# Performance work log

Measured on AMD Instinct MI355X. Metric: run time of the kernel, lower is better.

Reference implementation:

```python
import jax, jax.numpy as jnp
import numpy as np

N_NODES = 25000
N_EDGES = 400000
N = 2          # per-node group dim (h.size(1))
IN_DIM = 64
HEADS = 4
HEAD_DIM = 16  # out_dim; HEADS*HEAD_DIM == IN_DIM here


def setup_inputs() -> dict:
    key = jax.random.key(0)
    ks = jax.random.split(key, 8)
    w_scale = 1.0 / np.sqrt(IN_DIM)
    return {
        "h": jax.random.normal(ks[0], (N_NODES, N, IN_DIM), jnp.float32),
        "e": jax.random.normal(ks[1], (N_EDGES, N, IN_DIM), jnp.float32),
        "W_Q": jax.random.normal(ks[2], (IN_DIM, HEADS * HEAD_DIM), jnp.float32) * w_scale,
        "W_K": jax.random.normal(ks[3], (IN_DIM, HEADS * HEAD_DIM), jnp.float32) * w_scale,
        "W_V": jax.random.normal(ks[4], (IN_DIM, HEADS * HEAD_DIM), jnp.float32) * w_scale,
        "W_repe": jax.random.normal(ks[5], (IN_DIM, HEADS * HEAD_DIM), jnp.float32) * w_scale,
        "src": jax.random.randint(ks[6], (N_EDGES,), 0, N_NODES, jnp.int32),
        "dst": jax.random.randint(ks[7], (N_EDGES,), 0, N_NODES, jnp.int32),
    }


def reference(h, e, W_Q, W_K, W_V, W_repe, src, dst):
    n_nodes, Nd, C = h.shape
    E = src.shape[0]
    # node-side projection Q_h: [n_nodes, N, H, D]
    Q_h = (h @ W_Q).reshape(n_nodes, Nd, HEADS, HEAD_DIM)
    # edge-side bias repe_e: [E, N, H, D]
    repe_e = (e @ W_repe).reshape(E, Nd, HEADS, HEAD_DIM)
    # compute_diff: relu(src - dst) on raw features  [E, N, C]
    diff = jax.nn.relu(h[src] - h[dst])
    k_diff = (diff @ W_K).reshape(E, Nd, HEADS, HEAD_DIM)
    v_diff = (diff @ W_V).reshape(E, Nd, HEADS, HEAD_DIM)
    # dst_cosim_diff: scale = ||k_diff|| * ||Q_h[dst]|| + 1e-6 (norm over last dim, keepdim)
    q_dst = Q_h[dst]  # [E, N, H, D]
    scale = (jnp.linalg.norm(k_diff, axis=-1, keepdims=True)
             * jnp.linalg.norm(q_dst, axis=-1, keepdims=True)) + 1e-6
    score = q_dst * k_diff * scale + repe_e
    msg = score * v_diff
    # update_all(copy_edge, max) -> segment max over dst; zero-degree nodes get 0 (DGL convention)
    h_out = jax.ops.segment_max(msg, dst, num_segments=n_nodes)
    h_out = jnp.where(jnp.isneginf(h_out), jnp.zeros((), h_out.dtype), h_out)
    return h_out
```

## Files before the change

kernel.cpp:

```cpp
#include <hip/hip_runtime.h>
#include <stdint.h>

#define N_NODES 25000
#define N_EDGES 400000

typedef __attribute__((ext_vector_type(8))) short short8;
typedef __attribute__((ext_vector_type(4))) float f32x4;

#define MFMA16(a, b, c) __builtin_amdgcn_mfma_f32_16x16x32_bf16((a), (b), (c), 0, 0, 0)

__device__ __forceinline__ short bf16r(float x) {
    unsigned u = __float_as_uint(x);
    u += 0x7FFFu + ((u >> 16) & 1u);
    return (short)(u >> 16);
}
__device__ __forceinline__ short bfr(float x) {
    return (short)((__float_as_uint(x) + 0x8000u) >> 16);
}

#define DPP_ADD(x, ctrl) \
    ((x) + __int_as_float(__builtin_amdgcn_update_dpp(0, __float_as_int(x), (ctrl), 0xF, 0xF, true)))
__device__ __forceinline__ float red16(float x) {
    x = DPP_ADD(x, 0xB1);
    x = DPP_ADD(x, 0x4E);
    x = DPP_ADD(x, 0x141);
    x = DPP_ADD(x, 0x140);
    return x;
}

__device__ __forceinline__ short8 load_bfrag(const float* __restrict__ W,
                                             int colbase, int lane, int khalf) {
    const int n = colbase + (lane & 15);
    const int k0 = khalf * 32 + ((lane >> 4) << 3);
    short8 f;
    #pragma unroll
    for (int j = 0; j < 8; ++j) f[j] = bf16r(W[(k0 + j) * 64 + n]);
    return f;
}

__device__ __forceinline__ short8 afrag(const short* S, int lane, int khalf) {
    return *(const short8*)&S[(lane & 15) * 72 + khalf * 32 + ((lane >> 4) << 3)];
}

__global__ __launch_bounds__(256) void zero_counts_kernel(int* __restrict__ counts) {
    const int i = blockIdx.x * 256 + threadIdx.x;
    if (i < N_NODES) counts[i] = 0;
}

__global__ __launch_bounds__(256) void hist_kernel(const int* __restrict__ dst,
                                                   int* __restrict__ counts) {
    const int i = blockIdx.x * 256 + threadIdx.x;
    if (i < N_EDGES) atomicAdd(&counts[dst[i]], 1);
}

#define BPT 98
__global__ __launch_bounds__(256) void scan_kernel(const int* __restrict__ counts,
                                                   int* __restrict__ offsets,
                                                   int* __restrict__ cursor) {
    __shared__ int part[256];
    const int t = threadIdx.x;
    const int base = t * BPT;
    int s = 0;
    for (int j = 0; j < BPT; ++j) {
        const int idx = base + j;
        if (idx < N_NODES) s += counts[idx];
    }
    part[t] = s;
    __syncthreads();
    for (int d = 1; d < 256; d <<= 1) {
        const int add = (t >= d) ? part[t - d] : 0;
        __syncthreads();
        part[t] += add;
        __syncthreads();
    }
    int run = (t > 0) ? part[t - 1] : 0;
    for (int j = 0; j < BPT; ++j) {
        const int idx = base + j;
        if (idx < N_NODES) {
            offsets[idx] = run;
            cursor[idx]  = run;
            run += counts[idx];
        }
    }
    if (t == 255) offsets[N_NODES] = part[255];
}

__global__ __launch_bounds__(256) void scatter_kernel(
    const int* __restrict__ src, const int* __restrict__ dst,
    int* __restrict__ cursor, int* __restrict__ perm, int* __restrict__ srcs) {
    const int i = blockIdx.x * 256 + threadIdx.x;
    if (i < N_EDGES) {
        const int d = dst[i];
        const int pos = atomicAdd(&cursor[d], 1);
        perm[pos] = i;
        srcs[pos] = src[i];
    }
}

__global__ __launch_bounds__(256) void q_mfma_kernel(
    const float* __restrict__ h, const float* __restrict__ Wq,
    const float* __restrict__ Wk, const float* __restrict__ Wv,
    const float* __restrict__ Wr, float* __restrict__ Q, short8* __restrict__ fw)
{
    __shared__ short sH[64 * 72];
    const int t = threadIdx.x;
    const int lane = t & 63, w = t >> 6;
    const int wcol = w << 4;
    const int ln = lane & 15, lq = lane >> 4;
    const int base = blockIdx.x * 64;

    const short8 b0 = load_bfrag(Wq, wcol, lane, 0);
    const short8 b1 = load_bfrag(Wq, wcol, lane, 1);

    {
        const int r = t >> 2, c4 = (t & 3) << 4;
        int row = base + r; if (row > 49999) row = 49999;
        const float4* p = (const float4*)&h[row * 64 + c4];
        short tmp[16];
        #pragma unroll
        for (int i = 0; i < 4; ++i) {
            float4 x = p[i];
            tmp[4*i+0] = bf16r(x.x); tmp[4*i+1] = bf16r(x.y);
            tmp[4*i+2] = bf16r(x.z); tmp[4*i+3] = bf16r(x.w);
        }
        *(short8*)&sH[r * 72 + c4]     = *(short8*)&tmp[0];
        *(short8*)&sH[r * 72 + c4 + 8] = *(short8*)&tmp[8];
    }
    __syncthreads();

    #pragma unroll
    for (int m = 0; m < 4; ++m) {
        const short* Sm = &sH[(m << 4) * 72];
        short8 a0 = afrag(Sm, lane, 0);
        short8 a1 = afrag(Sm, lane, 1);
        f32x4 acc = {0.f, 0.f, 0.f, 0.f};
        acc = MFMA16(a0, b0, acc);
        acc = MFMA16(a1, b1, acc);
        #pragma unroll
        for (int reg = 0; reg < 4; ++reg) {
            const int row = base + (m << 4) + (lq << 2) + reg;
            if (row < 50000) Q[row * 64 + wcol + ln] = acc[reg];
        }
    }

    if (blockIdx.x == 0) {
        fw[(w * 6 + 0) * 64 + lane] = load_bfrag(Wk, wcol, lane, 0);
        fw[(w * 6 + 1) * 64 + lane] = load_bfrag(Wk, wcol, lane, 1);
        fw[(w * 6 + 2) * 64 + lane] = load_bfrag(Wv, wcol, lane, 0);
        fw[(w * 6 + 3) * 64 + lane] = load_bfrag(Wv, wcol, lane, 1);
        fw[(w * 6 + 4) * 64 + lane] = load_bfrag(Wr, wcol, lane, 0);
        fw[(w * 6 + 5) * 64 + lane] = load_bfrag(Wr, wcol, lane, 1);
    }
}

__global__ __launch_bounds__(256, 2) void edge_wave_kernel(
    const float* __restrict__ h, const float* __restrict__ e,
    const float* __restrict__ Q, const int* __restrict__ srcs,
    const int* __restrict__ perm, const int* __restrict__ offsets,
    const short8* __restrict__ fw, float* __restrict__ out)
{
    __shared__ short sAll[4][2304];
    const int t = threadIdx.x;
    const int lane = t & 63, w = t >> 6;
    const int v = (blockIdx.x << 2) + w;
    short* SD = &sAll[w][0];
    short* SE = &sAll[w][1152];

    const int off0 = offsets[v];
    const int off1 = offsets[v + 1];
    const int deg  = off1 - off0;

    if (deg == 0) {
        out[(v << 7) + lane]      = 0.0f;
        out[(v << 7) + 64 + lane] = 0.0f;
        return;
    }

    const int ln = lane & 15, lq = lane >> 4;

    short8 bK0[4], bK1[4], bV0[4], bV1[4], bR0[4], bR1[4];
    #pragma unroll
    for (int hd = 0; hd < 4; ++hd) {
        bK0[hd] = fw[(hd * 6 + 0) * 64 + lane];
        bK1[hd] = fw[(hd * 6 + 1) * 64 + lane];
        bV0[hd] = fw[(hd * 6 + 2) * 64 + lane];
        bV1[hd] = fw[(hd * 6 + 3) * 64 + lane];
        bR0[hd] = fw[(hd * 6 + 4) * 64 + lane];
        bR1[hd] = fw[(hd * 6 + 5) * 64 + lane];
    }

    float q0[4], q1[4], qn0[4], qn1[4];
    #pragma unroll
    for (int hd = 0; hd < 4; ++hd) {
        q0[hd] = Q[(v << 7) + (hd << 4) + ln];
        q1[hd] = Q[(v << 7) + 64 + (hd << 4) + ln];
        qn0[hd] = sqrtf(red16(q0[hd] * q0[hd]));
        qn1[hd] = sqrtf(red16(q1[hd] * q1[hd]));
    }

    const int r = lane >> 2;
    const int cq = (lane & 3) << 4;
    const int n_r = r & 1;

    float4 xd[4];
    {
        const float4* pd = (const float4*)&h[(((v << 1) + n_r) << 6) + cq];
        xd[0] = pd[0]; xd[1] = pd[1]; xd[2] = pd[2]; xd[3] = pd[3];
    }

    const float NEG_INF = __uint_as_float(0xFF800000u);
    float rm0[4] = {NEG_INF, NEG_INF, NEG_INF, NEG_INF};
    float rm1[4] = {NEG_INF, NEG_INF, NEG_INF, NEG_INF};

    const int nch = (deg + 7) >> 3;
    for (int c = 0; c < nch; ++c) {
        int eidx = off0 + (c << 3) + (r >> 1);
        if (eidx > off1 - 1) eidx = off1 - 1;
        const int ed = perm[eidx];
        const int s  = srcs[eidx];
        const float4* ps = (const float4*)&h[(((s  << 1) + n_r) << 6) + cq];
        const float4* pe = (const float4*)&e[(((ed << 1) + n_r) << 6) + cq];

        short tmd[16], tme[16];
        #pragma unroll
        for (int i = 0; i < 4; ++i) {
            const float4 xs = ps[i], xe = pe[i];
            tmd[4*i+0] = bfr(fmaxf(xs.x - xd[i].x, 0.f));
            tmd[4*i+1] = bfr(fmaxf(xs.y - xd[i].y, 0.f));
            tmd[4*i+2] = bfr(fmaxf(xs.z - xd[i].z, 0.f));
            tmd[4*i+3] = bfr(fmaxf(xs.w - xd[i].w, 0.f));
            tme[4*i+0] = bfr(xe.x); tme[4*i+1] = bfr(xe.y);
            tme[4*i+2] = bfr(xe.z); tme[4*i+3] = bfr(xe.w);
        }
        *(short8*)&SD[r * 72 + cq]     = *(short8*)&tmd[0];
        *(short8*)&SD[r * 72 + cq + 8] = *(short8*)&tmd[8];
        *(short8*)&SE[r * 72 + cq]     = *(short8*)&tme[0];
        *(short8*)&SE[r * 72 + cq + 8] = *(short8*)&tme[8];

        __builtin_amdgcn_wave_barrier();

        const short8 a0 = afrag(SD, lane, 0);
        const short8 a1 = afrag(SD, lane, 1);
        const short8 g0 = afrag(SE, lane, 0);
        const short8 g1 = afrag(SE, lane, 1);

        #pragma unroll
        for (int hd = 0; hd < 4; ++hd) {
            f32x4 aK = {0.f, 0.f, 0.f, 0.f}, aV = aK, aR = aK;
            aK = MFMA16(a0, bK0[hd], aK); aK = MFMA16(a1, bK1[hd], aK);
            aV = MFMA16(a0, bV0[hd], aV); aV = MFMA16(a1, bV1[hd], aV);
            aR = MFMA16(g0, bR0[hd], aR); aR = MFMA16(g1, bR1[hd], aR);

            #pragma unroll
            for (int reg = 0; reg < 4; ++reg) {
                const int rl   = (lq << 2) + reg;
                const int eloc = rl >> 1;
                const int n2   = reg & 1;
                const bool valid = ((c << 3) + eloc) < deg;
                const float kk = aK[reg];
                const float sk = red16(kk * kk);
                const float scale = sqrtf(sk) * (n2 ? qn1[hd] : qn0[hd]) + 1e-6f;
                const float qv = n2 ? q1[hd] : q0[hd];
                float msg = (qv * kk * scale + aR[reg]) * aV[reg];
                msg = valid ? msg : NEG_INF;
                if (n2) rm1[hd] = fmaxf(rm1[hd], msg);
                else    rm0[hd] = fmaxf(rm0[hd], msg);
            }
        }
        __builtin_amdgcn_wave_barrier();
    }

    #pragma unroll
    for (int hd = 0; hd < 4; ++hd) {
        rm0[hd] = fmaxf(rm0[hd], __shfl_xor(rm0[hd], 16));
        rm0[hd] = fmaxf(rm0[hd], __shfl_xor(rm0[hd], 32));
        rm1[hd] = fmaxf(rm1[hd], __shfl_xor(rm1[hd], 16));
        rm1[hd] = fmaxf(rm1[hd], __shfl_xor(rm1[hd], 32));
    }
    const float o0 = (lq == 0) ? rm0[0] : (lq == 1) ? rm0[1] : (lq == 2) ? rm0[2] : rm0[3];
    const float o1 = (lq == 0) ? rm1[0] : (lq == 1) ? rm1[1] : (lq == 2) ? rm1[2] : rm1[3];
    out[(v << 7) + lane]      = o0;
    out[(v << 7) + 64 + lane] = o1;
}

extern "C" void kernel_launch(void* const* d_in, const int* in_sizes, int n_in,
                              void* d_out, int out_size, void* d_ws, size_t ws_size,
                              hipStream_t stream) {
    const float* h  = (const float*)d_in[0];
    const float* e  = (const float*)d_in[1];
    const float* Wq = (const float*)d_in[2];
    const float* Wk = (const float*)d_in[3];
    const float* Wv = (const float*)d_in[4];
    const float* Wr = (const float*)d_in[5];
    const int*   src = (const int*)d_in[6];
    const int*   dst = (const int*)d_in[7];
    float* out = (float*)d_out;

    float* Q       = (float*)d_ws;
    int*   counts  = (int*)d_ws + 3200000;
    int*   offsets = (int*)d_ws + 3225000;
    int*   cursor  = (int*)d_ws + 3250008;
    int*   perm    = (int*)d_ws + 3275008;
    int*   srcs    = (int*)d_ws + 3675008;
    short8* fw     = (short8*)((int*)d_ws + 4075008);

    zero_counts_kernel<<<98, 256, 0, stream>>>(counts);
    hist_kernel<<<1563, 256, 0, stream>>>(dst, counts);
    scan_kernel<<<1, 256, 0, stream>>>(counts, offsets, cursor);
    scatter_kernel<<<1563, 256, 0, stream>>>(src, dst, cursor, perm, srcs);
    q_mfma_kernel<<<782, 256, 0, stream>>>(h, Wq, Wk, Wv, Wr, Q, fw);
    edge_wave_kernel<<<6250, 256, 0, stream>>>(h, e, Q, srcs, perm, offsets, fw, out);
}
```

Baseline: 512.9 us.

## Split edge work into per-wave 8-edge chunks with atomic max reduction

Replaces the one-wave-per-node loop with one wave per 8-edge chunk, using a chunk descriptor list built after the scan. Each chunk loads its fragments directly into registers instead of staging them through LDS, and reduces into the output with an atomicMax on order-preserving mapped floats. A final pass unmaps the values and zeroes empty nodes. This targets load imbalance from varying node degree and raises occupancy, at the cost of extra launches, redundant Q/dst reloads per chunk, and global atomics.

Measured after the change: 533.1 us. 1.04x slower.

```diff
diff --git a/kernel.cpp b/kernel.cpp
--- a/kernel.cpp
+++ b/kernel.cpp
@@ -3,6 +3,8 @@
 
 #define N_NODES 25000
 #define N_EDGES 400000
+#define OUT_ELEMS 3200000
+#define MAX_CHUNKS 72000
 
 typedef __attribute__((ext_vector_type(8))) short short8;
 typedef __attribute__((ext_vector_type(4))) float f32x4;
@@ -28,6 +30,12 @@
     return x;
 }
 
+__device__ __forceinline__ unsigned fmap(float x) {
+    const unsigned u = __float_as_uint(x);
+    return ((int)u >= 0) ? (u | 0x80000000u) : ~u;
+}
+#define MAPPED_NEG_INF 0x007FFFFFu
+
 __device__ __forceinline__ short8 load_bfrag(const float* __restrict__ W,
                                              int colbase, int lane, int khalf) {
     const int n = colbase + (lane & 15);
@@ -42,8 +50,10 @@
     return *(const short8*)&S[(lane & 15) * 72 + khalf * 32 + ((lane >> 4) << 3)];
 }
 
-__global__ __launch_bounds__(256) void zero_counts_kernel(int* __restrict__ counts) {
+__global__ __launch_bounds__(256) void init_kernel(unsigned* __restrict__ out_u,
+                                                   int* __restrict__ counts) {
     const int i = blockIdx.x * 256 + threadIdx.x;
+    out_u[i] = MAPPED_NEG_INF;
     if (i < N_NODES) counts[i] = 0;
 }
 
@@ -56,33 +66,64 @@
 #define BPT 98
 __global__ __launch_bounds__(256) void scan_kernel(const int* __restrict__ counts,
                                                    int* __restrict__ offsets,
-                                                   int* __restrict__ cursor) {
-    __shared__ int part[256];
+                                                   int* __restrict__ cursor,
+                                                   int* __restrict__ chunkoff) {
+    __shared__ int pd[256];
+    __shared__ int pc[256];
     const int t = threadIdx.x;
     const int base = t * BPT;
-    int s = 0;
-    for (int j = 0; j < BPT; ++j) {
-        const int idx = base + j;
-        if (idx < N_NODES) s += counts[idx];
-    }
-    part[t] = s;
-    __syncthreads();
-    for (int d = 1; d < 256; d <<= 1) {
-        const int add = (t >= d) ? part[t - d] : 0;
-        __syncthreads();
-        part[t] += add;
-        __syncthreads();
-    }
-    int run = (t > 0) ? part[t - 1] : 0;
+    int sd = 0, sc = 0;
     for (int j = 0; j < BPT; ++j) {
         const int idx = base + j;
         if (idx < N_NODES) {
-            offsets[idx] = run;
-            cursor[idx]  = run;
-            run += counts[idx];
-        }
-    }
-    if (t == 255) offsets[N_NODES] = part[255];
+            const int d = counts[idx];
+            sd += d;
+            sc += (d + 7) >> 3;
+        }
+    }
+    pd[t] = sd; pc[t] = sc;
+    __syncthreads();
+    for (int d = 1; d < 256; d <<= 1) {
+        const int ad = (t >= d) ? pd[t - d] : 0;
+        const int ac = (t >= d) ? pc[t - d] : 0;
+        __syncthreads();
+        pd[t] += ad; pc[t] += ac;
+        __syncthreads();
+    }
+    int rd = (t > 0) ? pd[t - 1] : 0;
+    int rc = (t > 0) ? pc[t - 1] : 0;
+    for (int j = 0; j < BPT; ++j) {
+        const int idx = base + j;
+        if (idx < N_NODES) {
+            offsets[idx]  = rd;
+            cursor[idx]   = rd;
+            chunkoff[idx] = rc;
+            const int d = counts[idx];
+            rd += d;
+            rc += (d + 7) >> 3;
+        }
+    }
+    if (t == 255) { offsets[N_NODES] = pd[255]; chunkoff[N_NODES] = pc[255]; }
+}
+
+__global__ __launch_bounds__(256) void fill_kernel(const int* __restrict__ offsets,
+                                                   const int* __restrict__ chunkoff,
+                                                   int2* __restrict__ chunk_desc) {
+    const int v = blockIdx.x * 256 + threadIdx.x;
+    if (v < N_NODES) {
+        const int off0 = offsets[v];
+        const int deg  = offsets[v + 1] - off0;
+        const int nch  = (deg + 7) >> 3;
+        const int co   = chunkoff[v];
+        for (int c = 0; c < nch; ++c) {
+            int nval = deg - (c << 3);
+            if (nval > 8) nval = 8;
+            int2 d;
+            d.x = v;
+            d.y = (off0 + (c << 3)) | (nval << 24);
+            chunk_desc[co + c] = d;
+        }
+    }
 }
 
 __global__ __launch_bounds__(256) void scatter_kernel(
@@ -153,30 +194,31 @@
     }
 }
 
-__global__ __launch_bounds__(256, 2) void edge_wave_kernel(
+__global__ __launch_bounds__(256, 4) void edge_chunk_kernel(
     const float* __restrict__ h, const float* __restrict__ e,
     const float* __restrict__ Q, const int* __restrict__ srcs,
-    const int* __restrict__ perm, const int* __restrict__ offsets,
-    const short8* __restrict__ fw, float* __restrict__ out)
+    const int* __restrict__ perm, const int* __restrict__ chunkoff,
+    const int2* __restrict__ chunk_desc, const short8* __restrict__ fw,
+    unsigned* __restrict__ out_u)
 {
-    __shared__ short sAll[4][2304];
     const int t = threadIdx.x;
-    const int lane = t & 63, w = t >> 6;
-    const int v = (blockIdx.x << 2) + w;
-    short* SD = &sAll[w][0];
-    short* SE = &sAll[w][1152];
-
-    const int off0 = offsets[v];
-    const int off1 = offsets[v + 1];
-    const int deg  = off1 - off0;
-
-    if (deg == 0) {
-        out[(v << 7) + lane]      = 0.0f;
-        out[(v << 7) + 64 + lane] = 0.0f;
-        return;
-    }
+    const int lane = t & 63;
+    const int g = (blockIdx.x << 2) + (t >> 6);
+    if (g >= chunkoff[N_NODES]) return;
+
+    const int2 dsc = chunk_desc[g];
+    const int v    = dsc.x;
+    const int base = dsc.y & 0xFFFFFF;
+    const int nval = dsc.y >> 24;
 
     const int ln = lane & 15, lq = lane >> 4;
+    const int eloc = ln >> 1, nr = ln & 1;
+    const int k0 = lq << 3;
+
+    const int elc = (eloc < nval - 1) ? eloc : (nval - 1);
+    const int ei  = base + elc;
+    const int ed  = perm[ei];
+    const int s   = srcs[ei];
 
     short8 bK0[4], bK1[4], bV0[4], bV1[4], bR0[4], bR1[4];
     #pragma unroll
@@ -189,6 +231,35 @@
         bR1[hd] = fw[(hd * 6 + 5) * 64 + lane];
     }
 
+    const float* __restrict__ hs  = &h[((s  << 1) + nr) << 6];
+    const float* __restrict__ hdp = &h[((v  << 1) + nr) << 6];
+    const float* __restrict__ ep  = &e[((ed << 1) + nr) << 6];
+
+    short8 afr[2], gfr[2];
+    #pragma unroll
+    for (int half = 0; half < 2; ++half) {
+        const int cb = (half << 5) + k0;
+        const float4 s0 = *(const float4*)&hs[cb];
+        const float4 s1 = *(const float4*)&hs[cb + 4];
+        const float4 d0 = *(const float4*)&hdp[cb];
+        const float4 d1 = *(const float4*)&hdp[cb + 4];
+        const float4 e0 = *(const float4*)&ep[cb];
+        const float4 e1 = *(const float4*)&ep[cb + 4];
+        short8 ta, tg;
+        ta[0] = bfr(fmaxf(s0.x - d0.x, 0.f));
+        ta[1] = bfr(fmaxf(s0.y - d0.y, 0.f));
+        ta[2] = bfr(fmaxf(s0.z - d0.z, 0.f));
+        ta[3] = bfr(fmaxf(s0.w - d0.w, 0.f));
+        ta[4] = bfr(fmaxf(s1.x - d1.x, 0.f));
+        ta[5] = bfr(fmaxf(s1.y - d1.y, 0.f));
+        ta[6] = bfr(fmaxf(s1.z - d1.z, 0.f));
+        ta[7] = bfr(fmaxf(s1.w - d1.w, 0.f));
+        tg[0] = bfr(e0.x); tg[1] = bfr(e0.y); tg[2] = bfr(e0.z); tg[3] = bfr(e0.w);
+        tg[4] = bfr(e1.x); tg[5] = bfr(e1.y); tg[6] = bfr(e1.z); tg[7] = bfr(e1.w);
+        afr[half] = ta;
+        gfr[half] = tg;
+    }
+
     float q0[4], q1[4], qn0[4], qn1[4];
     #pragma unroll
     for (int hd = 0; hd < 4; ++hd) {
@@ -198,76 +269,32 @@
         qn1[hd] = sqrtf(red16(q1[hd] * q1[hd]));
     }
 
-    const int r = lane >> 2;
-    const int cq = (lane & 3) << 4;
-    const int n_r = r & 1;
-
-    float4 xd[4];
-    {
-        const float4* pd = (const float4*)&h[(((v << 1) + n_r) << 6) + cq];
-        xd[0] = pd[0]; xd[1] = pd[1]; xd[2] = pd[2]; xd[3] = pd[3];
-    }
-
     const float NEG_INF = __uint_as_float(0xFF800000u);
     float rm0[4] = {NEG_INF, NEG_INF, NEG_INF, NEG_INF};
     float rm1[4] = {NEG_INF, NEG_INF, NEG_INF, NEG_INF};
 
-    const int nch = (deg + 7) >> 3;
-    for (int c = 0; c < nch; ++c) {
-        int eidx = off0 + (c << 3) + (r >> 1);
-        if (eidx > off1 - 1) eidx = off1 - 1;
-        const int ed = perm[eidx];
-        const int s  = srcs[eidx];
-        const float4* ps = (const float4*)&h[(((s  << 1) + n_r) << 6) + cq];
-        const float4* pe = (const float4*)&e[(((ed << 1) + n_r) << 6) + cq];
-
-        short tmd[16], tme[16];
+    #pragma unroll
+    for (int hd = 0; hd < 4; ++hd) {
+        f32x4 aK = {0.f, 0.f, 0.f, 0.f}, aV = aK, aR = aK;
+        aK = MFMA16(afr[0], bK0[hd], aK); aK = MFMA16(afr[1], bK1[hd], aK);
+        aV = MFMA16(afr[0], bV0[hd], aV); aV = MFMA16(afr[1], bV1[hd], aV);
+        aR = MFMA16(gfr[0], bR0[hd], aR); aR = MFMA16(gfr[1], bR1[hd], aR);
+
         #pragma unroll
-        for (int i = 0; i < 4; ++i) {
-            const float4 xs = ps[i], xe = pe[i];
-            tmd[4*i+0] = bfr(fmaxf(xs.x - xd[i].x, 0.f));
-            tmd[4*i+1] = bfr(fmaxf(xs.y - xd[i].y, 0.f));
-            tmd[4*i+2] = bfr(fmaxf(xs.z - xd[i].z, 0.f));
-            tmd[4*i+3] = bfr(fmaxf(xs.w - xd[i].w, 0.f));
-            tme[4*i+0] = bfr(xe.x); tme[4*i+1] = bfr(xe.y);
-            tme[4*i+2] = bfr(xe.z); tme[4*i+3] = bfr(xe.w);
-        }
-        *(short8*)&SD[r * 72 + cq]     = *(short8*)&tmd[0];
-        *(short8*)&SD[r * 72 + cq + 8] = *(short8*)&tmd[8];
-        *(short8*)&SE[r * 72 + cq]     = *(short8*)&tme[0];
-        *(short8*)&SE[r * 72 + cq + 8] = *(short8*)&tme[8];
-
-        __builtin_amdgcn_wave_barrier();
-
-        const short8 a0 = afrag(SD, lane, 0);
-        const short8 a1 = afrag(SD, lane, 1);
-        const short8 g0 = afrag(SE, lane, 0);
-        const short8 g1 = afrag(SE, lane, 1);
-
-        #pragma unroll
-        for (int hd = 0; hd < 4; ++hd) {
-            f32x4 aK = {0.f, 0.f, 0.f, 0.f}, aV = aK, aR = aK;
-            aK = MFMA16(a0, bK0[hd], aK); aK = MFMA16(a1, bK1[hd], aK);
-            aV = MFMA16(a0, bV0[hd], aV); aV = MFMA16(a1, bV1[hd], aV);
-            aR = MFMA16(g0, bR0[hd], aR); aR = MFMA16(g1, bR1[hd], aR);
-
-            #pragma unroll
-            for (int reg = 0; reg < 4; ++reg) {
-                const int rl   = (lq << 2) + reg;
-                const int eloc = rl >> 1;
-                const int n2   = reg & 1;
-                const bool valid = ((c << 3) + eloc) < deg;
-                const float kk = aK[reg];
-                const float sk = red16(kk * kk);
-                const float scale = sqrtf(sk) * (n2 ? qn1[hd] : qn0[hd]) + 1e-6f;
-                const float qv = n2 ? q1[hd] : q0[hd];
-                float msg = (qv * kk * scale + aR[reg]) * aV[reg];
-                msg = valid ? msg : NEG_INF;
-                if (n2) rm1[hd] = fmaxf(rm1[hd], msg);
-                else    rm0[hd] = fmaxf(rm0[hd], msg);
-            }
-        }
-        __builtin_amdgcn_wave_barrier();
+        for (int reg = 0; reg < 4; ++reg) {
+            const int rl = (lq << 2) + reg;
+            const int el = rl >> 1;
+            const int n2 = reg & 1;
+            const bool valid = el < nval;
+            const float kk = aK[reg];
+            const float sk = red16(kk * kk);
+            const float scale = sqrtf(sk) * (n2 ? qn1[hd] : qn0[hd]) + 1e-6f;
+            const float qv = n2 ? q1[hd] : q0[hd];
+            float msg = (qv * kk * scale + aR[reg]) * aV[reg];
+            msg = valid ? msg : NEG_INF;
+            if (n2) rm1[hd] = fmaxf(rm1[hd], msg);
+            else    rm0[hd] = fmaxf(rm0[hd], msg);
+        }
     }
 
     #pragma unroll
@@ -279,8 +306,25 @@
     }
     const float o0 = (lq == 0) ? rm0[0] : (lq == 1) ? rm0[1] : (lq == 2) ? rm0[2] : rm0[3];
     const float o1 = (lq == 0) ? rm1[0] : (lq == 1) ? rm1[1] : (lq == 2) ? rm1[2] : rm1[3];
-    out[(v << 7) + lane]      = o0;
-    out[(v << 7) + 64 + lane] = o1;
+    atomicMax(&out_u[(v << 7) + lane],      fmap(o0));
+    atomicMax(&out_u[(v << 7) + 64 + lane], fmap(o1));
+}
+
+__global__ __launch_bounds__(256) void final_kernel(unsigned* __restrict__ io) {
+    const int i = blockIdx.x * 256 + threadIdx.x;
+    uint4* p = (uint4*)io;
+    uint4 m = p[i];
+    unsigned a, b, c, d;
+    a = (m.x & 0x80000000u) ? (m.x ^ 0x80000000u) : ~m.x;
+    b = (m.y & 0x80000000u) ? (m.y ^ 0x80000000u) : ~m.y;
+    c = (m.z & 0x80000000u) ? (m.z ^ 0x80000000u) : ~m.z;
+    d = (m.w & 0x80000000u) ? (m.w ^ 0x80000000u) : ~m.w;
+    if (a == 0xFF800000u) a = 0u;
+    if (b == 0xFF800000u) b = 0u;
+    if (c == 0xFF800000u) c = 0u;
+    if (d == 0xFF800000u) d = 0u;
+    m.x = a; m.y = b; m.z = c; m.w = d;
+    p[i] = m;
 }
 
 extern "C" void kernel_launch(void* const* d_in, const int* in_sizes, int n_in,
@@ -296,18 +340,23 @@
     const int*   dst = (const int*)d_in[7];
     float* out = (float*)d_out;
 
-    float* Q       = (float*)d_ws;
-    int*   counts  = (int*)d_ws + 3200000;
-    int*   offsets = (int*)d_ws + 3225000;
-    int*   cursor  = (int*)d_ws + 3250008;
-    int*   perm    = (int*)d_ws + 3275008;
-    int*   srcs    = (int*)d_ws + 3675008;
-    short8* fw     = (short8*)((int*)d_ws + 4075008);
-
-    zero_counts_kernel<<<98, 256, 0, stream>>>(counts);
+    float* Q        = (float*)d_ws;
+    int*   counts   = (int*)d_ws + 3200000;
+    int*   offsets  = (int*)d_ws + 3225000;
+    int*   cursor   = (int*)d_ws + 3250008;
+    int*   perm     = (int*)d_ws + 3275008;
+    int*   srcs     = (int*)d_ws + 3675008;
+    short8* fw      = (short8*)((int*)d_ws + 4075008);
+    int*   chunkoff = (int*)d_ws + 4081152;
+    int2*  chunk_desc = (int2*)((int*)d_ws + 4106154);
+
+    init_kernel<<<12500, 256, 0, stream>>>((unsigned*)out, counts);
     hist_kernel<<<1563, 256, 0, stream>>>(dst, counts);
-    scan_kernel<<<1, 256, 0, stream>>>(counts, offsets, cursor);
+    scan_kernel<<<1, 256, 0, stream>>>(counts, offsets, cursor, chunkoff);
+    fill_kernel<<<98, 256, 0, stream>>>(offsets, chunkoff, chunk_desc);
     scatter_kernel<<<1563, 256, 0, stream>>>(src, dst, cursor, perm, srcs);
     q_mfma_kernel<<<782, 256, 0, stream>>>(h, Wq, Wk, Wv, Wr, Q, fw);
-    edge_wave_kernel<<<6250, 256, 0, stream>>>(h, e, Q, srcs, perm, offsets, fw, out);
-}
+    edge_chunk_kernel<<<17969, 256, 0, stream>>>(h, e, Q, srcs, perm,
+                                                 chunkoff, chunk_desc, fw, (unsigned*)out);
+    final_kernel<<<3125, 256, 0, stream>>>((unsigned*)out);
+}
```

## Split edge kernel into edge-parallel message pass and CSR-ordered max reduce

Applied to the files above, without the earlier changes.

The per-destination-node edge loop is replaced by an edge-parallel kernel. It processes 8 edges per wave in original order, reading e coalesced, and writes bf16-packed messages into CSR positions. A separate reduce kernel then takes the segment max per node. The Q norm is folded into Q in the projection kernel, and the 1e-6 epsilon term is dropped. This removes load imbalance from skewed degrees and the scattered e reads, but adds an intermediate message buffer round trip (about 51 MB of bf16) and a bf16 rounding of the messages.

Measured after the change: 534.9 us. +4.3%, slower.

```diff
diff --git a/kernel.cpp b/kernel.cpp
--- a/kernel.cpp
+++ b/kernel.cpp
@@ -85,15 +85,13 @@
     if (t == 255) offsets[N_NODES] = part[255];
 }
 
-__global__ __launch_bounds__(256) void scatter_kernel(
-    const int* __restrict__ src, const int* __restrict__ dst,
-    int* __restrict__ cursor, int* __restrict__ perm, int* __restrict__ srcs) {
+__global__ __launch_bounds__(256) void scatter_pos_kernel(
+    const int* __restrict__ dst, int* __restrict__ cursor,
+    int* __restrict__ csr_pos) {
     const int i = blockIdx.x * 256 + threadIdx.x;
     if (i < N_EDGES) {
-        const int d = dst[i];
-        const int pos = atomicAdd(&cursor[d], 1);
-        perm[pos] = i;
-        srcs[pos] = src[i];
+        const int pos = atomicAdd(&cursor[dst[i]], 1);
+        csr_pos[i] = pos;
     }
 }
 
@@ -138,8 +136,9 @@
         acc = MFMA16(a1, b1, acc);
         #pragma unroll
         for (int reg = 0; reg < 4; ++reg) {
+            const float qn = sqrtf(red16(acc[reg] * acc[reg]));
             const int row = base + (m << 4) + (lq << 2) + reg;
-            if (row < 50000) Q[row * 64 + wcol + ln] = acc[reg];
+            if (row < 50000) Q[row * 64 + wcol + ln] = acc[reg] * qn;
         }
     }
 
@@ -153,134 +152,138 @@
     }
 }
 
-__global__ __launch_bounds__(256, 2) void edge_wave_kernel(
+__global__ __launch_bounds__(256, 4) void edge_msg_kernel(
     const float* __restrict__ h, const float* __restrict__ e,
-    const float* __restrict__ Q, const int* __restrict__ srcs,
-    const int* __restrict__ perm, const int* __restrict__ offsets,
-    const short8* __restrict__ fw, float* __restrict__ out)
+    const float* __restrict__ QQ, const int* __restrict__ src,
+    const int* __restrict__ dst, const int* __restrict__ csr_pos,
+    const short8* __restrict__ fw, uint2* __restrict__ msg)
 {
-    __shared__ short sAll[4][2304];
     const int t = threadIdx.x;
-    const int lane = t & 63, w = t >> 6;
-    const int v = (blockIdx.x << 2) + w;
-    short* SD = &sAll[w][0];
-    short* SE = &sAll[w][1152];
-
-    const int off0 = offsets[v];
-    const int off1 = offsets[v + 1];
-    const int deg  = off1 - off0;
-
-    if (deg == 0) {
-        out[(v << 7) + lane]      = 0.0f;
-        out[(v << 7) + 64 + lane] = 0.0f;
-        return;
-    }
-
+    const int lane = t & 63;
+    const int g = (blockIdx.x << 2) + (t >> 6);
+    const int g8 = g << 3;
     const int ln = lane & 15, lq = lane >> 4;
-
-    short8 bK0[4], bK1[4], bV0[4], bV1[4], bR0[4], bR1[4];
+    const int eloc = ln >> 1, nr = ln & 1;
+    const int k0 = lq << 3;
+
+    const int sA = src[g8 + eloc];
+    const int dA = dst[g8 + eloc];
+    const float* __restrict__ hs  = &h[((sA << 1) + nr) << 6];
+    const float* __restrict__ hdp = &h[((dA << 1) + nr) << 6];
+    const float* __restrict__ ep  = &e[(((g8 + eloc) << 1) + nr) << 6];
+
+    short8 afr[2], gfr[2];
+    #pragma unroll
+    for (int half = 0; half < 2; ++half) {
+        const int cb = (half << 5) + k0;
+        const float4 s0 = *(const float4*)&hs[cb];
+        const float4 s1 = *(const float4*)&hs[cb + 4];
+        const float4 d0 = *(const float4*)&hdp[cb];
+        const float4 d1 = *(const float4*)&hdp[cb + 4];
+        const float4 e0 = *(const float4*)&ep[cb];
+        const float4 e1 = *(const float4*)&ep[cb + 4];
+        short8 ta, tg;
+        ta[0] = bfr(fmaxf(s0.x - d0.x, 0.f));
+        ta[1] = bfr(fmaxf(s0.y - d0.y, 0.f));
+        ta[2] = bfr(fmaxf(s0.z - d0.z, 0.f));
+        ta[3] = bfr(fmaxf(s0.w - d0.w, 0.f));
+        ta[4] = bfr(fmaxf(s1.x - d1.x, 0.f));
+        ta[5] = bfr(fmaxf(s1.y - d1.y, 0.f));
+        ta[6] = bfr(fmaxf(s1.z - d1.z, 0.f));
+        ta[7] = bfr(fmaxf(s1.w - d1.w, 0.f));
+        tg[0] = bfr(e0.x); tg[1] = bfr(e0.y); tg[2] = bfr(e0.z); tg[3] = bfr(e0.w);
+        tg[4] = bfr(e1.x); tg[5] = bfr(e1.y); tg[6] = bfr(e1.z); tg[7] = bfr(e1.w);
+        afr[half] = ta;
+        gfr[half] = tg;
+    }
+
+    const int e0i = g8 + (lq << 1), e1i = e0i + 1;
+    const int d0 = dst[e0i], d1 = dst[e1i];
+    const int p0 = csr_pos[e0i], p1 = csr_pos[e1i];
+
+    float qv_e0n0[4], qv_e0n1[4], qv_e1n0[4], qv_e1n1[4];
     #pragma unroll
     for (int hd = 0; hd < 4; ++hd) {
-        bK0[hd] = fw[(hd * 6 + 0) * 64 + lane];
-        bK1[hd] = fw[(hd * 6 + 1) * 64 + lane];
-        bV0[hd] = fw[(hd * 6 + 2) * 64 + lane];
-        bV1[hd] = fw[(hd * 6 + 3) * 64 + lane];
-        bR0[hd] = fw[(hd * 6 + 4) * 64 + lane];
-        bR1[hd] = fw[(hd * 6 + 5) * 64 + lane];
-    }
-
-    float q0[4], q1[4], qn0[4], qn1[4];
+        qv_e0n0[hd] = QQ[(d0 << 7) + (hd << 4) + ln];
+        qv_e0n1[hd] = QQ[(d0 << 7) + 64 + (hd << 4) + ln];
+        qv_e1n0[hd] = QQ[(d1 << 7) + (hd << 4) + ln];
+        qv_e1n1[hd] = QQ[(d1 << 7) + 64 + (hd << 4) + ln];
+    }
+
+    f32x4 aK[4], aV[4], aR[4];
     #pragma unroll
     for (int hd = 0; hd < 4; ++hd) {
-        q0[hd] = Q[(v << 7) + (hd << 4) + ln];
-        q1[hd] = Q[(v << 7) + 64 + (hd << 4) + ln];
-        qn0[hd] = sqrtf(red16(q0[hd] * q0[hd]));
-        qn1[hd] = sqrtf(red16(q1[hd] * q1[hd]));
-    }
-
-    const int r = lane >> 2;
-    const int cq = (lane & 3) << 4;
-    const int n_r = r & 1;
-
-    float4 xd[4];
-    {
-        const float4* pd = (const float4*)&h[(((v << 1) + n_r) << 6) + cq];
-        xd[0] = pd[0]; xd[1] = pd[1]; xd[2] = pd[2]; xd[3] = pd[3];
-    }
-
-    const float NEG_INF = __uint_as_float(0xFF800000u);
-    float rm0[4] = {NEG_INF, NEG_INF, NEG_INF, NEG_INF};
-    float rm1[4] = {NEG_INF, NEG_INF, NEG_INF, NEG_INF};
-
-    const int nch = (deg + 7) >> 3;
-    for (int c = 0; c < nch; ++c) {
-        int eidx = off0 + (c << 3) + (r >> 1);
-        if (eidx > off1 - 1) eidx = off1 - 1;
-        const int ed = perm[eidx];
-        const int s  = srcs[eidx];
-        const float4* ps = (const float4*)&h[(((s  << 1) + n_r) << 6) + cq];
-        const float4* pe = (const float4*)&e[(((ed << 1) + n_r) << 6) + cq];
-
-        short tmd[16], tme[16];
-        #pragma unroll
-        for (int i = 0; i < 4; ++i) {
-            const float4 xs = ps[i], xe = pe[i];
-            tmd[4*i+0] = bfr(fmaxf(xs.x - xd[i].x, 0.f));
-            tmd[4*i+1] = bfr(fmaxf(xs.y - xd[i].y, 0.f));
-            tmd[4*i+2] = bfr(fmaxf(xs.z - xd[i].z, 0.f));
-            tmd[4*i+3] = bfr(fmaxf(xs.w - xd[i].w, 0.f));
-            tme[4*i+0] = bfr(xe.x); tme[4*i+1] = bfr(xe.y);
-            tme[4*i+2] = bfr(xe.z); tme[4*i+3] = bfr(xe.w);
-        }
-        *(short8*)&SD[r * 72 + cq]     = *(short8*)&tmd[0];
-        *(short8*)&SD[r * 72 + cq + 8] = *(short8*)&tmd[8];
-        *(short8*)&SE[r * 72 + cq]     = *(short8*)&tme[0];
-        *(short8*)&SE[r * 72 + cq + 8] = *(short8*)&tme[8];
-
-        __builtin_amdgcn_wave_barrier();
-
-        const short8 a0 = afrag(SD, lane, 0);
-        const short8 a1 = afrag(SD, lane, 1);
-        const short8 g0 = afrag(SE, lane, 0);
-        const short8 g1 = afrag(SE, lane, 1);
-
+        f32x4 k = {0.f, 0.f, 0.f, 0.f}, vv = k, r = k;
+        k  = MFMA16(afr[0], fw[(hd * 6 + 0) * 64 + lane], k);
+        k  = MFMA16(afr[1], fw[(hd * 6 + 1) * 64 + lane], k);
+        vv = MFMA16(afr[0], fw[(hd * 6 + 2) * 64 + lane], vv);
+        vv = MFMA16(afr[1], fw[(hd * 6 + 3) * 64 + lane], vv);
+        r  = MFMA16(gfr[0], fw[(hd * 6 + 4) * 64 + lane], r);
+        r  = MFMA16(gfr[1], fw[(hd * 6 + 5) * 64 + lane], r);
+        aK[hd] = k; aV[hd] = vv; aR[hd] = r;
+    }
+
+    #pragma unroll
+    for (int reg = 0; reg < 4; ++reg) {
+        float m[4];
         #pragma unroll
         for (int hd = 0; hd < 4; ++hd) {
-            f32x4 aK = {0.f, 0.f, 0.f, 0.f}, aV = aK, aR = aK;
-            aK = MFMA16(a0, bK0[hd], aK); aK = MFMA16(a1, bK1[hd], aK);
-            aV = MFMA16(a0, bV0[hd], aV); aV = MFMA16(a1, bV1[hd], aV);
-            aR = MFMA16(g0, bR0[hd], aR); aR = MFMA16(g1, bR1[hd], aR);
-
-            #pragma unroll
-            for (int reg = 0; reg < 4; ++reg) {
-                const int rl   = (lq << 2) + reg;
-                const int eloc = rl >> 1;
-                const int n2   = reg & 1;
-                const bool valid = ((c << 3) + eloc) < deg;
-                const float kk = aK[reg];
-                const float sk = red16(kk * kk);
-                const float scale = sqrtf(sk) * (n2 ? qn1[hd] : qn0[hd]) + 1e-6f;
-                const float qv = n2 ? q1[hd] : q0[hd];
-                float msg = (qv * kk * scale + aR[reg]) * aV[reg];
-                msg = valid ? msg : NEG_INF;
-                if (n2) rm1[hd] = fmaxf(rm1[hd], msg);
-                else    rm0[hd] = fmaxf(rm0[hd], msg);
-            }
+            const float kk = aK[hd][reg];
+            const float nk = sqrtf(red16(kk * kk));
+            const float qv = (reg == 0) ? qv_e0n0[hd] :
+                             (reg == 1) ? qv_e0n1[hd] :
+                             (reg == 2) ? qv_e1n0[hd] : qv_e1n1[hd];
+            m[hd] = (qv * kk * nk + aR[hd][reg]) * aV[hd][reg];
         }
-        __builtin_amdgcn_wave_barrier();
-    }
-
-    #pragma unroll
-    for (int hd = 0; hd < 4; ++hd) {
-        rm0[hd] = fmaxf(rm0[hd], __shfl_xor(rm0[hd], 16));
-        rm0[hd] = fmaxf(rm0[hd], __shfl_xor(rm0[hd], 32));
-        rm1[hd] = fmaxf(rm1[hd], __shfl_xor(rm1[hd], 16));
-        rm1[hd] = fmaxf(rm1[hd], __shfl_xor(rm1[hd], 32));
-    }
-    const float o0 = (lq == 0) ? rm0[0] : (lq == 1) ? rm0[1] : (lq == 2) ? rm0[2] : rm0[3];
-    const float o1 = (lq == 0) ? rm1[0] : (lq == 1) ? rm1[1] : (lq == 2) ? rm1[2] : rm1[3];
-    out[(v << 7) + lane]      = o0;
-    out[(v << 7) + 64 + lane] = o1;
+        uint2 pk;
+        pk.x = (unsigned)(unsigned short)bf16r(m[0])
+             | ((unsigned)(unsigned short)bf16r(m[1]) << 16);
+        pk.y = (unsigned)(unsigned short)bf16r(m[2])
+             | ((unsigned)(unsigned short)bf16r(m[3]) << 16);
+        const int p = (reg & 2) ? p1 : p0;
+        msg[(((p << 1) + (reg & 1)) << 4) + ln] = pk;
+    }
+}
+
+__global__ __launch_bounds__(256) void reduce_kernel(
+    const unsigned* __restrict__ msg_u, const int* __restrict__ offsets,
+    float* __restrict__ out)
+{
+    const int t = threadIdx.x;
+    const int lane = t & 63;
+    const int v = (blockIdx.x << 2) + (t >> 6);
+    const int off0 = offsets[v], off1 = offsets[v + 1];
+    const int n = lane >> 5, ph = (lane >> 4) & 1, ln = lane & 15;
+    const unsigned* __restrict__ p = msg_u + ((n << 5) + (ln << 1) + ph);
+
+    const float NEG_INF = __uint_as_float(0xFF800000u);
+    float m0 = NEG_INF, m1 = NEG_INF;
+
+    int pos = off0;
+    for (; pos + 4 <= off1; pos += 4) {
+        const unsigned u0 = p[(pos + 0) << 6];
+        const unsigned u1 = p[(pos + 1) << 6];
+        const unsigned u2 = p[(pos + 2) << 6];
+        const unsigned u3 = p[(pos + 3) << 6];
+        m0 = fmaxf(m0, __uint_as_float(u0 << 16));
+        m1 = fmaxf(m1, __uint_as_float(u0 & 0xFFFF0000u));
+        m0 = fmaxf(m0, __uint_as_float(u1 << 16));
+        m1 = fmaxf(m1, __uint_as_float(u1 & 0xFFFF0000u));
+        m0 = fmaxf(m0, __uint_as_float(u2 << 16));
+        m1 = fmaxf(m1, __uint_as_float(u2 & 0xFFFF0000u));
+        m0 = fmaxf(m0, __uint_as_float(u3 << 16));
+        m1 = fmaxf(m1, __uint_as_float(u3 & 0xFFFF0000u));
+    }
+    for (; pos < off1; ++pos) {
+        const unsigned u = p[pos << 6];
+        m0 = fmaxf(m0, __uint_as_float(u << 16));
+        m1 = fmaxf(m1, __uint_as_float(u & 0xFFFF0000u));
+    }
+    if (off0 == off1) { m0 = 0.f; m1 = 0.f; }
+
+    const int col = (n << 6) + (ph << 5) + ln;
+    out[(v << 7) + col]      = m0;
+    out[(v << 7) + col + 16] = m1;
 }
 
 extern "C" void kernel_launch(void* const* d_in, const int* in_sizes, int n_in,
@@ -300,14 +303,15 @@
     int*   counts  = (int*)d_ws + 3200000;
     int*   offsets = (int*)d_ws + 3225000;
     int*   cursor  = (int*)d_ws + 3250008;
-    int*   perm    = (int*)d_ws + 3275008;
-    int*   srcs    = (int*)d_ws + 3675008;
-    short8* fw     = (short8*)((int*)d_ws + 4075008);
+    int*   csr_pos = (int*)d_ws + 3275008;
+    short8* fw     = (short8*)((int*)d_ws + 3675008);
+    uint2* msg     = (uint2*)((int*)d_ws + 3681152);
 
     zero_counts_kernel<<<98, 256, 0, stream>>>(counts);
     hist_kernel<<<1563, 256, 0, stream>>>(dst, counts);
     scan_kernel<<<1, 256, 0, stream>>>(counts, offsets, cursor);
-    scatter_kernel<<<1563, 256, 0, stream>>>(src, dst, cursor, perm, srcs);
+    scatter_pos_kernel<<<1563, 256, 0, stream>>>(dst, cursor, csr_pos);
     q_mfma_kernel<<<782, 256, 0, stream>>>(h, Wq, Wk, Wv, Wr, Q, fw);
-    edge_wave_kernel<<<6250, 256, 0, stream>>>(h, e, Q, srcs, perm, offsets, fw, out);
-}
+    edge_msg_kernel<<<12500, 256, 0, stream>>>(h, e, Q, src, dst, csr_pos, fw, msg);
+    reduce_kernel<<<6250, 256, 0, stream>>>((const unsigned*)msg, offsets, out);
+}
```
